# Kernel optimization log

Hardware: AMD Instinct MI355X
Metric: run time of the kernel (lower is better)

Reference implementation:

```python
import jax, jax.numpy as jnp
import numpy as np

K = 10
NEG_SLOPE = 0.2


def _knn(x, k):
    # x: (B, C, N) -> idx (B, N, k) of k nearest neighbors (smallest sq-dist)
    inner = -2.0 * jnp.einsum('bcn,bcm->bnm', x, x)
    xx = jnp.sum(x * x, axis=1)  # (B, N)
    pd = -xx[:, :, None] - inner - xx[:, None, :]  # negative squared distance
    return jax.lax.top_k(pd, k)[1]


def _gather(xt, idx):
    # xt: (B, N, C), idx: (B, N, k) -> (B, N, k, C)
    return jax.vmap(lambda f, i: f[i])(xt, idx)


def graph_feature(x, k):
    # x: (B, C, N) -> (B, 2C, N, k)
    idx = _knn(x, k)
    xt = jnp.transpose(x, (0, 2, 1))  # (B, N, C)
    feat = _gather(xt, idx)           # (B, N, k, C)
    xc = xt[:, :, None, :]
    out = jnp.concatenate([feat - xc, jnp.broadcast_to(xc, feat.shape)], axis=3)
    return jnp.transpose(out, (0, 3, 1, 2))


def graph_feature1(x, k):
    # knn on first 2 dims (2D coords); x: (B, C, N) -> (B, 2C, N, k)
    idx = _knn(x[:, 0:2, :], k)
    xt = jnp.transpose(x, (0, 2, 1))
    feat = _gather(xt, idx)
    xc = jnp.broadcast_to(xt[:, :, None, :], feat.shape)
    out = jnp.concatenate([feat[..., :2] - xc[..., :2], feat[..., 2:], xc], axis=3)
    return jnp.transpose(out, (0, 3, 1, 2))


def _lrelu(v):
    return jnp.where(v >= 0, v, NEG_SLOPE * v)


def _cbr2(f, W, s, t):
    # 1x1 conv2d + folded-BN + leaky relu; f: (B, C, N, k)
    y = jnp.einsum('oc,bcnk->bonk', W, f)
    return _lrelu(y * s[None, :, None, None] + t[None, :, None, None])


def _cbr1(f, W, s, t):
    # 1x1 conv1d + folded-BN + leaky relu; f: (B, C, N)
    y = jnp.einsum('oc,bcn->bon', W, f)
    return _lrelu(y * s[None, :, None] + t[None, :, None])


def setup_inputs() -> dict:
    key = jax.random.key(0)
    ks = jax.random.split(key, 32)
    B, C, N = 8, 7, 4096
    d = {'x': jax.random.normal(ks[0], (B, C, N), jnp.float32)}
    wshapes = [('W1', (64, 14)), ('W2', (64, 64)), ('W3', (64, 128)), ('W4', (64, 64)),
               ('W5', (64, 128)), ('W6', (256, 192)), ('W7', (512, 448)), ('W8', (128, 1024))]
    for i, (n, s) in enumerate(wshapes):
        d[n] = jax.random.normal(ks[1 + i], s, jnp.float32) * (1.0 / np.sqrt(s[1]))
    bdims = [64, 64, 64, 64, 64, 256, 512, 128]
    for i, c in enumerate(bdims):
        d[f's{i + 1}'] = jax.random.uniform(ks[9 + i], (c,), jnp.float32, 0.5, 1.5)
        d[f't{i + 1}'] = jax.random.normal(ks[17 + i], (c,), jnp.float32) * 0.1
    return d


def reference(x, W1, W2, W3, W4, W5, W6, W7, W8,
              s1, s2, s3, s4, s5, s6, s7, s8,
              t1, t2, t3, t4, t5, t6, t7, t8):
    B, _, N = x.shape
    h = graph_feature1(x, K)              # (B, 14, N, K)
    h = _cbr2(h, W1, s1, t1)
    h = _cbr2(h, W2, s2, t2)
    x1 = h.mean(axis=-1)                  # (B, 64, N)
    h = graph_feature(x1, K)              # (B, 128, N, K)
    h = _cbr2(h, W3, s3, t3)
    h = _cbr2(h, W4, s4, t4)
    x2 = h.mean(axis=-1)
    h = graph_feature(x2, K)
    h = _cbr2(h, W5, s5, t5)
    x3 = h.mean(axis=-1)
    h = jnp.concatenate([x1, x2, x3], axis=1)   # (B, 192, N)
    h = _cbr1(h, W6, s6, t6)                    # (B, 256, N)
    g = h.mean(axis=-1, keepdims=True)          # (B, 256, 1)
    g = jnp.broadcast_to(g, (B, 256, N))
    h = jnp.concatenate([g, x1, x2, x3], axis=1)  # (B, 448, N)
    h = _cbr1(h, W7, s7, t7)                      # (B, 512, N)
    x4 = h.max(axis=-1)
    x5 = h.mean(axis=-1)
    h = jnp.concatenate([x4, x5], axis=1)         # (B, 1024)
    h = h @ W8.T                                  # (B, 128)
    return _lrelu(h * s8[None, :] + t8[None, :])
```

## Files before the change

kernel.cpp:

```cpp
#include <hip/hip_runtime.h>

#define BB 8
#define NN 4096
#define KK 10
#define CAP 24
#define TT 6
typedef unsigned long long u64;
typedef __attribute__((ext_vector_type(8))) short bf16x8;
typedef __attribute__((ext_vector_type(4))) float f32x4;

__device__ __forceinline__ float lrelu(float v){ return v >= 0.f ? v : 0.2f*v; }
__device__ __forceinline__ float bc(float v, int l){
  return __int_as_float(__builtin_amdgcn_readlane(__float_as_int(v), l));
}
__device__ __forceinline__ unsigned fenc(float f){
  unsigned u = __float_as_uint(f);
  return u ^ (((unsigned)((int)u >> 31)) | 0x80000000u);
}
__device__ __forceinline__ float fdec(unsigned e){
  return (e & 0x80000000u) ? __uint_as_float(e & 0x7fffffffu) : __uint_as_float(~e);
}
__device__ __forceinline__ u64 shflx_u64(u64 x, int d){
  unsigned lo = __shfl_xor((unsigned)x, d, 64);
  unsigned hi = __shfl_xor((unsigned)(x >> 32), d, 64);
  return ((u64)hi << 32) | lo;
}

__global__ __launch_bounds__(256) void prep_k(
    const float* __restrict__ W1, const float* __restrict__ W2, const float* __restrict__ W3,
    const float* __restrict__ W4, const float* __restrict__ W5, const float* __restrict__ W8,
    float* __restrict__ W1T, float* __restrict__ W2T, float* __restrict__ W3T,
    float* __restrict__ W4T, float* __restrict__ W5T, float* __restrict__ W8T)
{
  const int t = blockIdx.x*256 + threadIdx.x;
  const int stride = gridDim.x*256;
  for (int i=t; i<64*14; i+=stride){ int o=i/14, c=i%14; W1T[c*64+o]=W1[i]; }
  for (int i=t; i<64*64; i+=stride){ int o=i>>6, c=i&63; W2T[c*64+o]=W2[i]; }
  for (int i=t; i<64*128; i+=stride){ int o=i>>7, c=i&127; W3T[c*64+o]=W3[i]; }
  for (int i=t; i<64*64; i+=stride){ int o=i>>6, c=i&63; W4T[c*64+o]=W4[i]; }
  for (int i=t; i<64*128; i+=stride){ int o=i>>7, c=i&127; W5T[c*64+o]=W5[i]; }
  for (int i=t; i<128*1024; i+=stride){ int o=i>>10, c=i&1023; W8T[c*128+o]=W8[i]; }
}

__global__ __launch_bounds__(256) void cvt_k(const float* __restrict__ xin,
    unsigned short* __restrict__ Xh, unsigned short* __restrict__ Xl, float* __restrict__ xx)
{
  const int gid = blockIdx.x*256 + threadIdx.x;
  const int p = gid >> 3, c8 = (gid & 7) << 3;
  const float* src = xin + (size_t)p*64 + c8;
  float fv[8];
  *(float4*)&fv[0] = *(const float4*)(src);
  *(float4*)&fv[4] = *(const float4*)(src + 4);
  unsigned hp[4], lp[4];
  float ssq = 0.f;
  #pragma unroll
  for (int e=0; e<4; e++){
    float f0 = fv[2*e], f1 = fv[2*e+1];
    ssq += f0*f0 + f1*f1;
    unsigned u0 = __float_as_uint(f0), u1 = __float_as_uint(f1);
    hp[e] = (u0 >> 16) | (u1 & 0xffff0000u);
    float l0 = f0 - __uint_as_float(u0 & 0xffff0000u);
    float l1 = f1 - __uint_as_float(u1 & 0xffff0000u);
    lp[e] = (__float_as_uint(l0) >> 16) | (__float_as_uint(l1) & 0xffff0000u);
  }
  *(uint4*)(Xh + (size_t)p*64 + c8) = uint4{hp[0],hp[1],hp[2],hp[3]};
  *(uint4*)(Xl + (size_t)p*64 + c8) = uint4{lp[0],lp[1],lp[2],lp[3]};
  ssq += __shfl_xor(ssq, 1, 64);
  ssq += __shfl_xor(ssq, 2, 64);
  ssq += __shfl_xor(ssq, 4, 64);
  if ((gid & 7) == 0) xx[p] = ssq;
}

__global__ __launch_bounds__(256) void knn2d_k(const float* __restrict__ x, u64* __restrict__ pk)
{
  __shared__ float px[1024], py[1024], pxx[1024];
  __shared__ unsigned cnt[64];
  __shared__ u64 lst[64][CAP];
  const int tid = threadIdx.x;
  const int b  = blockIdx.x >> 8;
  const int qt = (blockIdx.x >> 2) & 63;
  const int h  = blockIdx.x & 3;
  const int q0 = qt*64;
  const int m0g = h*1024;
  const float* xb = x + (size_t)b*7*NN;
  for (int m = tid; m < 1024; m += 256){
    float a = xb[m0g + m], c = xb[NN + m0g + m];
    px[m] = a; py[m] = c; pxx[m] = a*a + c*c;
  }
  if (tid < 64) cnt[tid] = 0;
  __syncthreads();

  const int ty = tid >> 4, tx = tid & 15;
  const int qr = ty*4;
  float qx4[4], qy4[4], q24[4];
  #pragma unroll
  for (int i=0;i<4;i++){
    float a = xb[q0+qr+i], c = xb[NN + q0+qr+i];
    qx4[i] = a; qy4[i] = c; q24[i] = a*a + c*c;
  }

  float bv[4][TT];
  #pragma unroll
  for (int i=0;i<4;i++){
    #pragma unroll
    for (int s=0;s<TT;s++) bv[i][s] = -__builtin_inff();
  }

  for (int ot=0; ot<8; ot++){
    #pragma unroll
    for (int j=0;j<8;j++){
      const int ml = ot*128 + j*16 + tx;
      const float cmx = px[ml], cmy = py[ml], cm2 = pxx[ml];
      #pragma unroll
      for (int i=0;i<4;i++){
        float dot = qx4[i]*cmx + qy4[i]*cmy;
        float v = (-q24[i]) - (-2.f*dot) - cm2;
        float c = v;
        #pragma unroll
        for (int s=0;s<TT;s++){
          float nb = fmaxf(bv[i][s], c);
          c = fminf(bv[i][s], c);
          bv[i][s] = nb;
        }
      }
    }
  }

  float thr[4];
  #pragma unroll
  for (int i=0;i<4;i++){
    float m = 0.f;
    #pragma unroll
    for (int k=0;k<10;k++){
      float hh = bv[i][0];
      m = hh;
      m = fmaxf(m, __shfl_xor(m, 1, 64));
      m = fmaxf(m, __shfl_xor(m, 2, 64));
      m = fmaxf(m, __shfl_xor(m, 4, 64));
      m = fmaxf(m, __shfl_xor(m, 8, 64));
      if (k < 9){
        if (hh == m){
          #pragma unroll
          for (int s=0;s<TT-1;s++) bv[i][s] = bv[i][s+1];
          bv[i][TT-1] = -__builtin_inff();
        }
      }
    }
    thr[i] = m;
  }

  for (int ot=0; ot<8; ot++){
    #pragma unroll
    for (int j=0;j<8;j++){
      const int ml = ot*128 + j*16 + tx;
      const float cmx = px[ml], cmy = py[ml], cm2 = pxx[ml];
      const unsigned mk = ~(unsigned)(m0g + ml);
      #pragma unroll
      for (int i=0;i<4;i++){
        float dot = qx4[i]*cmx + qy4[i]*cmy;
        float v = (-q24[i]) - (-2.f*dot) - cm2;
        if (v >= thr[i]){
          u64 key = ((u64)fenc(v) << 32) | mk;
          const int r = qr + i;
          unsigned slot = atomicAdd(&cnt[r], 1u);
          if (slot < CAP) lst[r][slot] = key;
        }
      }
    }
  }
  __syncthreads();

  if (tid < 64){
    int n = (int)cnt[tid]; if (n > CAP) n = CAP;
    u64* L = lst[tid];
    u64* op = pk + (((size_t)b*NN + q0 + tid)*4 + h)*KK;
    for (int k=0;k<KK;k++){
      u64 best = 0ull; int bi = 0;
      for (int s=0;s<n;s++){
        u64 v2 = L[s];
        if (v2 > best){ best = v2; bi = s; }
      }
      if (best) L[bi] = 0ull;
      op[k] = best;
    }
  }
}

__global__ __launch_bounds__(256) void knn64_k(const unsigned short* __restrict__ Xh,
    const unsigned short* __restrict__ Xl, const float* __restrict__ xx, u64* __restrict__ pk)
{
  __shared__ unsigned short Ch[64*72], Cl[64*72];
  __shared__ float cxx[64];
  __shared__ unsigned cnt[64];
  __shared__ u64 lst[64][CAP];
  const int tid = threadIdx.x;
  const int b  = blockIdx.x >> 8;
  const int qt = (blockIdx.x >> 2) & 63;
  const int h  = blockIdx.x & 3;
  const int q0 = qt*64;
  const int m0g = h*1024;
  const unsigned short* Xhb = Xh + (size_t)b*NN*64;
  const unsigned short* Xlb = Xl + (size_t)b*NN*64;
  const float* xxb = xx + (size_t)b*NN;

  const int sp = tid >> 2;
  const int sc = (tid & 3) << 4;

  const int lane = tid & 63;
  const int w    = tid >> 6;
  const int col  = lane & 15;
  const int quad = (tid >> 4) & 3;
  const int qr   = (tid >> 4)*4;

  const size_t abase = (size_t)(q0 + w*16 + col)*64 + quad*8;
  bf16x8 Ah0 = *(const bf16x8*)(Xhb + abase);
  bf16x8 Ah1 = *(const bf16x8*)(Xhb + abase + 32);
  bf16x8 Al0 = *(const bf16x8*)(Xlb + abase);
  bf16x8 Al1 = *(const bf16x8*)(Xlb + abase + 32);

  float qx4[4];
  #pragma unroll
  for (int i=0;i<4;i++) qx4[i] = xxb[q0 + qr + i];

  if (tid < 64) cnt[tid] = 0;

  float bv[4][TT];
  #pragma unroll
  for (int i=0;i<4;i++){
    #pragma unroll
    for (int s=0;s<TT;s++) bv[i][s] = -__builtin_inff();
  }

  for (int ct=0; ct<16; ct++){
    const int m0 = m0g + ct*64;
    __syncthreads();
    {
      const uint4* sh = (const uint4*)(Xhb + (size_t)(m0+sp)*64 + sc);
      const uint4* sl = (const uint4*)(Xlb + (size_t)(m0+sp)*64 + sc);
      uint4 h0 = sh[0], h1 = sh[1], l0 = sl[0], l1 = sl[1];
      *(uint4*)(&Ch[sp*72 + sc])     = h0;
      *(uint4*)(&Ch[sp*72 + sc + 8]) = h1;
      *(uint4*)(&Cl[sp*72 + sc])     = l0;
      *(uint4*)(&Cl[sp*72 + sc + 8]) = l1;
      if (tid < 64) cxx[tid] = xxb[m0 + tid];
    }
    __syncthreads();

    #pragma unroll
    for (int j=0;j<4;j++){
      const int boff = (j*16 + col)*72 + quad*8;
      bf16x8 Bh0 = *(const bf16x8*)(&Ch[boff]);
      bf16x8 Bh1 = *(const bf16x8*)(&Ch[boff+32]);
      bf16x8 Bl0 = *(const bf16x8*)(&Cl[boff]);
      bf16x8 Bl1 = *(const bf16x8*)(&Cl[boff+32]);
      f32x4 d = {0.f,0.f,0.f,0.f};
      d = __builtin_amdgcn_mfma_f32_16x16x32_bf16(Al0, Bh0, d, 0,0,0);
      d = __builtin_amdgcn_mfma_f32_16x16x32_bf16(Ah0, Bl0, d, 0,0,0);
      d = __builtin_amdgcn_mfma_f32_16x16x32_bf16(Ah0, Bh0, d, 0,0,0);
      d = __builtin_amdgcn_mfma_f32_16x16x32_bf16(Al1, Bh1, d, 0,0,0);
      d = __builtin_amdgcn_mfma_f32_16x16x32_bf16(Ah1, Bl1, d, 0,0,0);
      d = __builtin_amdgcn_mfma_f32_16x16x32_bf16(Ah1, Bh1, d, 0,0,0);

      const float cx = cxx[j*16 + col];
      #pragma unroll
      for (int i=0;i<4;i++){
        float v = (-qx4[i]) - (-2.f*d[i]) - cx;
        float c = v;
        #pragma unroll
        for (int s=0;s<TT;s++){
          float nb = fmaxf(bv[i][s], c);
          c = fminf(bv[i][s], c);
          bv[i][s] = nb;
        }
      }
    }
  }

  float thr[4];
  #pragma unroll
  for (int i=0;i<4;i++){
    float m = 0.f;
    #pragma unroll
    for (int k=0;k<10;k++){
      float hh = bv[i][0];
      m = hh;
      m = fmaxf(m, __shfl_xor(m, 1, 64));
      m = fmaxf(m, __shfl_xor(m, 2, 64));
      m = fmaxf(m, __shfl_xor(m, 4, 64));
      m = fmaxf(m, __shfl_xor(m, 8, 64));
      if (k < 9){
        if (hh == m){
          #pragma unroll
          for (int s=0;s<TT-1;s++) bv[i][s] = bv[i][s+1];
          bv[i][TT-1] = -__builtin_inff();
        }
      }
    }
    thr[i] = m;
  }

  for (int ct=0; ct<16; ct++){
    const int m0 = m0g + ct*64;
    __syncthreads();
    {
      const uint4* sh = (const uint4*)(Xhb + (size_t)(m0+sp)*64 + sc);
      const uint4* sl = (const uint4*)(Xlb + (size_t)(m0+sp)*64 + sc);
      uint4 h0 = sh[0], h1 = sh[1], l0 = sl[0], l1 = sl[1];
      *(uint4*)(&Ch[sp*72 + sc])     = h0;
      *(uint4*)(&Ch[sp*72 + sc + 8]) = h1;
      *(uint4*)(&Cl[sp*72 + sc])     = l0;
      *(uint4*)(&Cl[sp*72 + sc + 8]) = l1;
      if (tid < 64) cxx[tid] = xxb[m0 + tid];
    }
    __syncthreads();

    #pragma unroll
    for (int j=0;j<4;j++){
      const int boff = (j*16 + col)*72 + quad*8;
      bf16x8 Bh0 = *(const bf16x8*)(&Ch[boff]);
      bf16x8 Bh1 = *(const bf16x8*)(&Ch[boff+32]);
      bf16x8 Bl0 = *(const bf16x8*)(&Cl[boff]);
      bf16x8 Bl1 = *(const bf16x8*)(&Cl[boff+32]);
      f32x4 d = {0.f,0.f,0.f,0.f};
      d = __builtin_amdgcn_mfma_f32_16x16x32_bf16(Al0, Bh0, d, 0,0,0);
      d = __builtin_amdgcn_mfma_f32_16x16x32_bf16(Ah0, Bl0, d, 0,0,0);
      d = __builtin_amdgcn_mfma_f32_16x16x32_bf16(Ah0, Bh0, d, 0,0,0);
      d = __builtin_amdgcn_mfma_f32_16x16x32_bf16(Al1, Bh1, d, 0,0,0);
      d = __builtin_amdgcn_mfma_f32_16x16x32_bf16(Ah1, Bl1, d, 0,0,0);
      d = __builtin_amdgcn_mfma_f32_16x16x32_bf16(Ah1, Bh1, d, 0,0,0);

      const int m = m0 + j*16 + col;
      const float cx = cxx[j*16 + col];
      const unsigned mk = ~(unsigned)m;
      #pragma unroll
      for (int i=0;i<4;i++){
        float v = (-qx4[i]) - (-2.f*d[i]) - cx;
        if (v >= thr[i]){
          u64 key = ((u64)fenc(v) << 32) | mk;
          const int r = qr + i;
          unsigned slot = atomicAdd(&cnt[r], 1u);
          if (slot < CAP) lst[r][slot] = key;
        }
      }
    }
  }
  __syncthreads();

  if (tid < 64){
    int n = (int)cnt[tid]; if (n > CAP) n = CAP;
    u64* L = lst[tid];
    u64* op = pk + (((size_t)b*NN + q0 + tid)*4 + h)*KK;
    for (int k=0;k<KK;k++){
      u64 best = 0ull; int bi = 0;
      for (int s=0;s<n;s++){
        u64 v2 = L[s];
        if (v2 > best){ best = v2; bi = s; }
      }
      if (best) L[bi] = 0ull;
      op[k] = best;
    }
  }
}

__global__ __launch_bounds__(256) void kmerge_k(const u64* __restrict__ pk, int* __restrict__ idxo)
{
  const int q = blockIdx.x*256 + threadIdx.x;
  const u64* A = pk + (size_t)q*(4*KK);
  int* op = idxo + (size_t)q*KK;
  int ia = 0, ib = 0, ic = 0, id = 0;
  #pragma unroll
  for (int k=0;k<KK;k++){
    u64 a  = (ia < KK) ? A[ia]        : 0ull;
    u64 b2 = (ib < KK) ? A[KK + ib]   : 0ull;
    u64 c2 = (ic < KK) ? A[2*KK + ic] : 0ull;
    u64 d2 = (id < KK) ? A[3*KK + id] : 0ull;
    u64 m1 = a >= b2 ? a : b2;  int s1 = a >= b2 ? 0 : 1;
    u64 m2 = c2 >= d2 ? c2 : d2; int s2 = c2 >= d2 ? 2 : 3;
    u64 mm = m1 >= m2 ? m1 : m2; int ss = m1 >= m2 ? s1 : s2;
    op[k] = (int)(~(unsigned)mm);
    if (ss == 0) ia++; else if (ss == 1) ib++; else if (ss == 2) ic++; else id++;
  }
}

__global__ __launch_bounds__(256) void edge1_k(const float* __restrict__ x, const int* __restrict__ idx,
    const float* __restrict__ W1T, const float* __restrict__ W2T,
    const float* __restrict__ s1, const float* __restrict__ t1,
    const float* __restrict__ s2, const float* __restrict__ t2,
    float* __restrict__ x1t)
{
  const int lane = threadIdx.x & 63;
  const int pt = (blockIdx.x << 2) + (threadIdx.x >> 6);
  const int b = pt >> 12, n = pt & 4095;
  const float* xb = x + (size_t)b*7*NN;
  float w1r[14], w2r[64];
  #pragma unroll
  for (int c=0;c<14;c++) w1r[c] = W1T[c*64 + lane];
  #pragma unroll
  for (int c=0;c<64;c++) w2r[c] = W2T[c*64 + lane];
  const float s1o=s1[lane], t1o=t1[lane], s2o=s2[lane], t2o=t2[lane];
  const float xq = (lane < 7) ? xb[lane*NN + n] : 0.f;
  const float xq0 = bc(xq,0), xq1 = bc(xq,1);
  float qy1 = 0.f;
  #pragma unroll
  for (int c=0;c<7;c++) qy1 += w1r[7+c]*bc(xq,c);
  const int* ip = idx + (size_t)pt*KK;
  float acc = 0.f;
  for (int j=0;j<KK;j++){
    const int ij = ip[j];
    const float xg = (lane < 7) ? xb[lane*NN + ij] : 0.f;
    float y1 = qy1;
    y1 += w1r[0]*(bc(xg,0) - xq0);
    y1 += w1r[1]*(bc(xg,1) - xq1);
    #pragma unroll
    for (int c=2;c<7;c++) y1 += w1r[c]*bc(xg,c);
    const float z1 = lrelu(y1*s1o + t1o);
    float p0=0.f,p1=0.f,p2=0.f,p3=0.f;
    #pragma unroll
    for (int c=0;c<64;c+=4){
      p0 += w2r[c+0]*bc(z1,c+0);
      p1 += w2r[c+1]*bc(z1,c+1);
      p2 += w2r[c+2]*bc(z1,c+2);
      p3 += w2r[c+3]*bc(z1,c+3);
    }
    acc += lrelu(((p0+p1)+(p2+p3))*s2o + t2o);
  }
  x1t[(size_t)pt*64 + lane] = acc / 10.f;
}

__global__ __launch_bounds__(256) void edge2_k(const float* __restrict__ xin, const int* __restrict__ idx,
    const float* __restrict__ W3T, const float* __restrict__ W4T,
    const float* __restrict__ s3, const float* __restrict__ t3,
    const float* __restrict__ s4, const float* __restrict__ t4,
    float* __restrict__ xout)
{
  const int lane = threadIdx.x & 63;
  const int pt = (blockIdx.x << 2) + (threadIdx.x >> 6);
  const int b = pt >> 12;
  float wd[64], wq[64], w4[64];
  #pragma unroll
  for (int c=0;c<64;c++) wd[c] = W3T[c*64 + lane];
  #pragma unroll
  for (int c=0;c<64;c++) wq[c] = W3T[(64+c)*64 + lane];
  #pragma unroll
  for (int c=0;c<64;c++) w4[c] = W4T[c*64 + lane];
  const float s3o=s3[lane], t3o=t3[lane], s4o=s4[lane], t4o=t4[lane];
  const float xq = xin[(size_t)pt*64 + lane];
  float a0=0.f,a1=0.f,a2=0.f,a3=0.f;
  #pragma unroll
  for (int c=0;c<64;c+=4){
    a0 += wq[c+0]*bc(xq,c+0);
    a1 += wq[c+1]*bc(xq,c+1);
    a2 += wq[c+2]*bc(xq,c+2);
    a3 += wq[c+3]*bc(xq,c+3);
  }
  const float yq = (a0+a1)+(a2+a3);
  const int* ip = idx + (size_t)pt*KK;
  float acc = 0.f;
  for (int j=0;j<KK;j++){
    const int ij = ip[j];
    const float xg = xin[((size_t)(b*NN + ij))*64 + lane];
    const float d = xg - xq;
    float p0=0.f,p1=0.f,p2=0.f,p3=0.f;
    #pragma unroll
    for (int c=0;c<64;c+=4){
      p0 += wd[c+0]*bc(d,c+0);
      p1 += wd[c+1]*bc(d,c+1);
      p2 += wd[c+2]*bc(d,c+2);
      p3 += wd[c+3]*bc(d,c+3);
    }
    const float z3 = lrelu((yq + ((p0+p1)+(p2+p3)))*s3o + t3o);
    float q0=0.f,q1=0.f,q2=0.f,q3=0.f;
    #pragma unroll
    for (int c=0;c<64;c+=4){
      q0 += w4[c+0]*bc(z3,c+0);
      q1 += w4[c+1]*bc(z3,c+1);
      q2 += w4[c+2]*bc(z3,c+2);
      q3 += w4[c+3]*bc(z3,c+3);
    }
    acc += lrelu(((q0+q1)+(q2+q3))*s4o + t4o);
  }
  xout[(size_t)pt*64 + lane] = acc / 10.f;
}

__global__ __launch_bounds__(256) void edge3_k(const float* __restrict__ xin, const int* __restrict__ idx,
    const float* __restrict__ W5T,
    const float* __restrict__ s5, const float* __restrict__ t5,
    float* __restrict__ xout)
{
  const int lane = threadIdx.x & 63;
  const int pt = (blockIdx.x << 2) + (threadIdx.x >> 6);
  const int b = pt >> 12;
  float wd[64], wq[64];
  #pragma unroll
  for (int c=0;c<64;c++) wd[c] = W5T[c*64 + lane];
  #pragma unroll
  for (int c=0;c<64;c++) wq[c] = W5T[(64+c)*64 + lane];
  const float s5o=s5[lane], t5o=t5[lane];
  const float xq = xin[(size_t)pt*64 + lane];
  float a0=0.f,a1=0.f,a2=0.f,a3=0.f;
  #pragma unroll
  for (int c=0;c<64;c+=4){
    a0 += wq[c+0]*bc(xq,c+0);
    a1 += wq[c+1]*bc(xq,c+1);
    a2 += wq[c+2]*bc(xq,c+2);
    a3 += wq[c+3]*bc(xq,c+3);
  }
  const float yq = (a0+a1)+(a2+a3);
  const int* ip = idx + (size_t)pt*KK;
  float acc = 0.f;
  for (int j=0;j<KK;j++){
    const int ij = ip[j];
    const float xg = xin[((size_t)(b*NN + ij))*64 + lane];
    const float d = xg - xq;
    float p0=0.f,p1=0.f,p2=0.f,p3=0.f;
    #pragma unroll
    for (int c=0;c<64;c+=4){
      p0 += wd[c+0]*bc(d,c+0);
      p1 += wd[c+1]*bc(d,c+1);
      p2 += wd[c+2]*bc(d,c+2);
      p3 += wd[c+3]*bc(d,c+3);
    }
    acc += lrelu((yq + ((p0+p1)+(p2+p3)))*s5o + t5o);
  }
  xout[(size_t)pt*64 + lane] = acc / 10.f;
}

__global__ __launch_bounds__(256) void g1_k(const float* __restrict__ W6,
   const float* __restrict__ x1t, const float* __restrict__ x2t, const float* __restrict__ x3t,
   const float* __restrict__ s6, const float* __restrict__ t6, float* __restrict__ gsum)
{
  __shared__ float Wl[16*132];
  __shared__ float Zl[16*260];
  const int tid = threadIdx.x;
  const int rb = blockIdx.x & 1;
  const int nt = (blockIdx.x >> 1) & 15;
  const int b  = blockIdx.x >> 5;
  const int r0 = rb*128;
  const int n0 = nt*256;
  const int ty = tid >> 4, tx = tid & 15;
  float acc[8][16];
  #pragma unroll
  for (int i=0;i<8;i++){
    #pragma unroll
    for (int j=0;j<16;j++) acc[i][j] = 0.f;
  }
  for (int kc=0; kc<12; kc++){
    __syncthreads();
    {
      const int r = tid >> 1, h = tid & 1;
      const float4* wp = (const float4*)(W6 + (size_t)(r0 + r)*192 + kc*16 + h*8);
      float tmp[8];
      *(float4*)&tmp[0] = wp[0];
      *(float4*)&tmp[4] = wp[1];
      #pragma unroll
      for (int u=0;u<8;u++) Wl[(h*8+u)*132 + r] = tmp[u];
    }
    {
      const float* arr = (kc < 4) ? x1t : (kc < 8) ? x2t : x3t;
      const int chofs = (kc & 3)*16;
      const float4* zp = (const float4*)(arr + ((size_t)(b*NN) + n0 + tid)*64 + chofs);
      float tmp[16];
      *(float4*)&tmp[0]  = zp[0];
      *(float4*)&tmp[4]  = zp[1];
      *(float4*)&tmp[8]  = zp[2];
      *(float4*)&tmp[12] = zp[3];
      #pragma unroll
      for (int u=0;u<16;u++) Zl[u*260 + tid] = tmp[u];
    }
    __syncthreads();
    #pragma unroll 4
    for (int k=0;k<16;k++){
      float wv[8], zv[16];
      *(float4*)&wv[0] = *(const float4*)(&Wl[k*132 + ty*8]);
      *(float4*)&wv[4] = *(const float4*)(&Wl[k*132 + ty*8 + 4]);
      #pragma unroll
      for (int jg=0;jg<4;jg++)
        *(float4*)&zv[jg*4] = *(const float4*)(&Zl[k*260 + jg*64 + tx*4]);
      #pragma unroll
      for (int i=0;i<8;i++){
        #pragma unroll
        for (int j=0;j<16;j++) acc[i][j] += wv[i]*zv[j];
      }
    }
  }
  #pragma unroll
  for (int i=0;i<8;i++){
    const int row = r0 + ty*8 + i;
    const float sv = s6[row], tv = t6[row];
    float sum = 0.f;
    #pragma unroll
    for (int j=0;j<16;j++) sum += lrelu(acc[i][j]*sv + tv);
    #pragma unroll
    for (int d=1; d<16; d<<=1) sum += __shfl_xor(sum, d, 64);
    if ((tid & 15) == 0) atomicAdd(&gsum[b*256 + row], sum);
  }
}

__global__ __launch_bounds__(256) void g2_k(const float* __restrict__ W7,
   const float* __restrict__ gsum, float* __restrict__ c7)
{
  const int b = blockIdx.x >> 1;
  const int o = (blockIdx.x & 1)*256 + threadIdx.x;
  const float* wr = W7 + (size_t)o*448;
  const float* gb = gsum + b*256;
  float a0=0.f,a1=0.f,a2=0.f,a3=0.f;
  #pragma unroll 4
  for (int c=0;c<256;c+=4){
    a0 += wr[c+0]*gb[c+0]; a1 += wr[c+1]*gb[c+1];
    a2 += wr[c+2]*gb[c+2]; a3 += wr[c+3]*gb[c+3];
  }
  c7[b*512+o] = ((a0+a1)+(a2+a3)) * (1.f/4096.f);
}

__global__ __launch_bounds__(256) void g3_k(const float* __restrict__ W7,
   const float* __restrict__ x1t, const float* __restrict__ x2t, const float* __restrict__ x3t,
   const float* __restrict__ c7, const float* __restrict__ s7, const float* __restrict__ t7,
   unsigned* __restrict__ x4e, float* __restrict__ x5s)
{
  __shared__ float Wl[16*132];
  __shared__ float Zl[16*260];
  const int tid = threadIdx.x;
  const int rb = blockIdx.x & 3;
  const int nt = (blockIdx.x >> 2) & 15;
  const int b  = blockIdx.x >> 6;
  const int r0 = rb*128;
  const int n0 = nt*256;
  const int ty = tid >> 4, tx = tid & 15;
  float acc[8][16];
  #pragma unroll
  for (int i=0;i<8;i++){
    #pragma unroll
    for (int j=0;j<16;j++) acc[i][j] = 0.f;
  }
  for (int kc=0; kc<12; kc++){
    __syncthreads();
    {
      const int r = tid >> 1, h = tid & 1;
      const float4* wp = (const float4*)(W7 + (size_t)(r0 + r)*448 + 256 + kc*16 + h*8);
      float tmp[8];
      *(float4*)&tmp[0] = wp[0];
      *(float4*)&tmp[4] = wp[1];
      #pragma unroll
      for (int u=0;u<8;u++) Wl[(h*8+u)*132 + r] = tmp[u];
    }
    {
      const float* arr = (kc < 4) ? x1t : (kc < 8) ? x2t : x3t;
      const int chofs = (kc & 3)*16;
      const float4* zp = (const float4*)(arr + ((size_t)(b*NN) + n0 + tid)*64 + chofs);
      float tmp[16];
      *(float4*)&tmp[0]  = zp[0];
      *(float4*)&tmp[4]  = zp[1];
      *(float4*)&tmp[8]  = zp[2];
      *(float4*)&tmp[12] = zp[3];
      #pragma unroll
      for (int u=0;u<16;u++) Zl[u*260 + tid] = tmp[u];
    }
    __syncthreads();
    #pragma unroll 4
    for (int k=0;k<16;k++){
      float wv[8], zv[16];
      *(float4*)&wv[0] = *(const float4*)(&Wl[k*132 + ty*8]);
      *(float4*)&wv[4] = *(const float4*)(&Wl[k*132 + ty*8 + 4]);
      #pragma unroll
      for (int jg=0;jg<4;jg++)
        *(float4*)&zv[jg*4] = *(const float4*)(&Zl[k*260 + jg*64 + tx*4]);
      #pragma unroll
      for (int i=0;i<8;i++){
        #pragma unroll
        for (int j=0;j<16;j++) acc[i][j] += wv[i]*zv[j];
      }
    }
  }
  #pragma unroll
  for (int i=0;i<8;i++){
    const int row = r0 + ty*8 + i;
    const float c7v = c7[b*512 + row];
    const float sv = s7[row], tv = t7[row];
    float mx = -__builtin_inff(), sum = 0.f;
    #pragma unroll
    for (int j=0;j<16;j++){
      float h = lrelu((acc[i][j] + c7v)*sv + tv);
      mx = fmaxf(mx, h); sum += h;
    }
    #pragma unroll
    for (int d=1; d<16; d<<=1){
      sum += __shfl_xor(sum, d, 64);
      mx = fmaxf(mx, __shfl_xor(mx, d, 64));
    }
    if ((tid & 15) == 0){
      atomicAdd(&x5s[b*512 + row], sum);
      atomicMax(&x4e[b*512 + row], fenc(mx));
    }
  }
}

__global__ __launch_bounds__(128) void g4_k(const float* __restrict__ W8T,
  const unsigned* __restrict__ x4e, const float* __restrict__ x5s,
  const float* __restrict__ s8, const float* __restrict__ t8, float* __restrict__ out)
{
  const int b = blockIdx.x, j = threadIdx.x;
  float a0 = 0.f, a1 = 0.f;
  for (int o=0;o<512;o++){
    a0 += W8T[o*128 + j] * fdec(x4e[b*512 + o]);
    a1 += W8T[(512+o)*128 + j] * (x5s[b*512 + o] * (1.f/4096.f));
  }
  const float y = a0 + a1;
  out[b*128 + j] = lrelu(y*s8[j] + t8[j]);
}

extern "C" void kernel_launch(void* const* d_in, const int* in_sizes, int n_in,
                              void* d_out, int out_size, void* d_ws, size_t ws_size,
                              hipStream_t stream) {
  (void)in_sizes; (void)n_in; (void)out_size; (void)ws_size;
  const float* x  = (const float*)d_in[0];
  const float* W1 = (const float*)d_in[1];
  const float* W2 = (const float*)d_in[2];
  const float* W3 = (const float*)d_in[3];
  const float* W4 = (const float*)d_in[4];
  const float* W5 = (const float*)d_in[5];
  const float* W6 = (const float*)d_in[6];
  const float* W7 = (const float*)d_in[7];
  const float* W8 = (const float*)d_in[8];
  const float* s1 = (const float*)d_in[9];   const float* t1 = (const float*)d_in[10];
  const float* s2 = (const float*)d_in[11];  const float* t2 = (const float*)d_in[12];
  const float* s3 = (const float*)d_in[13];  const float* t3 = (const float*)d_in[14];
  const float* s4 = (const float*)d_in[15];  const float* t4 = (const float*)d_in[16];
  const float* s5 = (const float*)d_in[17];  const float* t5 = (const float*)d_in[18];
  const float* s6 = (const float*)d_in[19];  const float* t6 = (const float*)d_in[20];
  const float* s7 = (const float*)d_in[21];  const float* t7 = (const float*)d_in[22];
  const float* s8 = (const float*)d_in[23];  const float* t8 = (const float*)d_in[24];

  char* wsb = (char*)d_ws;
  size_t off = 0;
  auto alloc = [&](size_t bytes)->char* {
    char* p = wsb + off;
    off += (bytes + 255) & ~(size_t)255;
    return p;
  };
  int*      idx1 = (int*)alloc((size_t)BB*NN*KK*4);
  int*      idx2 = (int*)alloc((size_t)BB*NN*KK*4);
  int*      idx3 = (int*)alloc((size_t)BB*NN*KK*4);
  u64*      pkeys= (u64*)alloc((size_t)BB*NN*4*KK*8);
  float*    x1t  = (float*)alloc((size_t)BB*NN*64*4);
  float*    x2t  = (float*)alloc((size_t)BB*NN*64*4);
  float*    x3t  = (float*)alloc((size_t)BB*NN*64*4);
  unsigned short* Xh = (unsigned short*)alloc((size_t)BB*NN*64*2);
  unsigned short* Xl = (unsigned short*)alloc((size_t)BB*NN*64*2);
  float*    xxb  = (float*)alloc((size_t)BB*NN*4);
  float*    gsum = (float*)alloc((size_t)BB*256*4);
  unsigned* x4e  = (unsigned*)alloc((size_t)BB*512*4);
  float*    x5s  = (float*)alloc((size_t)BB*512*4);
  float*    c7   = (float*)alloc((size_t)BB*512*4);
  float*    W1T  = (float*)alloc(14*64*4);
  float*    W2T  = (float*)alloc(64*64*4);
  float*    W3T  = (float*)alloc(128*64*4);
  float*    W4T  = (float*)alloc(64*64*4);
  float*    W5T  = (float*)alloc(128*64*4);
  float*    W8T  = (float*)alloc(1024*128*4);

  prep_k<<<64,256,0,stream>>>(W1,W2,W3,W4,W5,W8, W1T,W2T,W3T,W4T,W5T,W8T);
  knn2d_k<<<BB*64*4,256,0,stream>>>(x, pkeys);
  kmerge_k<<<BB*NN/256,256,0,stream>>>(pkeys, idx1);
  edge1_k<<<BB*NN/4,256,0,stream>>>(x, idx1, W1T, W2T, s1,t1,s2,t2, x1t);
  cvt_k<<<BB*NN*8/256,256,0,stream>>>(x1t, Xh, Xl, xxb);
  knn64_k<<<BB*64*4,256,0,stream>>>(Xh, Xl, xxb, pkeys);
  kmerge_k<<<BB*NN/256,256,0,stream>>>(pkeys, idx2);
  edge2_k<<<BB*NN/4,256,0,stream>>>(x1t, idx2, W3T, W4T, s3,t3,s4,t4, x2t);
  cvt_k<<<BB*NN*8/256,256,0,stream>>>(x2t, Xh, Xl, xxb);
  knn64_k<<<BB*64*4,256,0,stream>>>(Xh, Xl, xxb, pkeys);
  kmerge_k<<<BB*NN/256,256,0,stream>>>(pkeys, idx3);
  edge3_k<<<BB*NN/4,256,0,stream>>>(x2t, idx3, W5T, s5,t5, x3t);
  hipMemsetAsync(gsum, 0, (size_t)BB*256*4 + (size_t)BB*512*4*2, stream);
  g1_k<<<256,256,0,stream>>>(W6, x1t,x2t,x3t, s6,t6, gsum);
  g2_k<<<16,256,0,stream>>>(W7, gsum, c7);
  g3_k<<<512,256,0,stream>>>(W7, x1t,x2t,x3t, c7, s7,t7, x4e, x5s);
  g4_k<<<BB,128,0,stream>>>(W8T, x4e, x5s, s8,t8, (float*)d_out);
}
```

Baseline: 1.126 ms.

## Rewrite edge2 kernel with split-bf16 MFMA matmuls over 8-point tiles

Replaces the per-lane scalar FMA and readlane broadcast loops in edge2 with MFMA 16x16x32 bf16 matrix multiplies. Weights and gathered edge features are split into high and low bf16 parts (three products each) to keep accuracy close to fp32. Each block now handles 8 points (80 edges) staged in shared memory, and the per-point mean is formed with shared-memory atomics. This removes the 192-float per-thread weight registers and the scalar work, at the cost of LDS traffic, extra barriers and a small loss of precision from dropping the low-times-low term.

```diff
diff --git a/kernel.cpp b/kernel.cpp
--- a/kernel.cpp
+++ b/kernel.cpp
@@ -29,17 +29,40 @@
 __global__ __launch_bounds__(256) void prep_k(
     const float* __restrict__ W1, const float* __restrict__ W2, const float* __restrict__ W3,
     const float* __restrict__ W4, const float* __restrict__ W5, const float* __restrict__ W8,
-    float* __restrict__ W1T, float* __restrict__ W2T, float* __restrict__ W3T,
-    float* __restrict__ W4T, float* __restrict__ W5T, float* __restrict__ W8T)
+    float* __restrict__ W1T, float* __restrict__ W2T, float* __restrict__ W5T, float* __restrict__ W8T,
+    unsigned short* __restrict__ W3dh, unsigned short* __restrict__ W3dl,
+    unsigned short* __restrict__ W3qh, unsigned short* __restrict__ W3ql,
+    unsigned short* __restrict__ W4h,  unsigned short* __restrict__ W4l)
 {
   const int t = blockIdx.x*256 + threadIdx.x;
   const int stride = gridDim.x*256;
   for (int i=t; i<64*14; i+=stride){ int o=i/14, c=i%14; W1T[c*64+o]=W1[i]; }
   for (int i=t; i<64*64; i+=stride){ int o=i>>6, c=i&63; W2T[c*64+o]=W2[i]; }
-  for (int i=t; i<64*128; i+=stride){ int o=i>>7, c=i&127; W3T[c*64+o]=W3[i]; }
-  for (int i=t; i<64*64; i+=stride){ int o=i>>6, c=i&63; W4T[c*64+o]=W4[i]; }
   for (int i=t; i<64*128; i+=stride){ int o=i>>7, c=i&127; W5T[c*64+o]=W5[i]; }
   for (int i=t; i<128*1024; i+=stride){ int o=i>>10, c=i&1023; W8T[c*128+o]=W8[i]; }
+  for (int i=t; i<64*64; i+=stride){
+    int o=i>>6, c=i&63;
+    float f = W3[o*128 + c];
+    unsigned u = __float_as_uint(f);
+    W3dh[i] = (unsigned short)(u >> 16);
+    float lo = f - __uint_as_float(u & 0xffff0000u);
+    W3dl[i] = (unsigned short)(__float_as_uint(lo) >> 16);
+  }
+  for (int i=t; i<64*64; i+=stride){
+    int o=i>>6, c=i&63;
+    float f = W3[o*128 + 64 + c];
+    unsigned u = __float_as_uint(f);
+    W3qh[i] = (unsigned short)(u >> 16);
+    float lo = f - __uint_as_float(u & 0xffff0000u);
+    W3ql[i] = (unsigned short)(__float_as_uint(lo) >> 16);
+  }
+  for (int i=t; i<64*64; i+=stride){
+    float f = W4[i];
+    unsigned u = __float_as_uint(f);
+    W4h[i] = (unsigned short)(u >> 16);
+    float lo = f - __uint_as_float(u & 0xffff0000u);
+    W4l[i] = (unsigned short)(__float_as_uint(lo) >> 16);
+  }
 }
 
 __global__ __launch_bounds__(256) void cvt_k(const float* __restrict__ xin,
@@ -427,59 +450,206 @@
   x1t[(size_t)pt*64 + lane] = acc / 10.f;
 }
 
-__global__ __launch_bounds__(256) void edge2_k(const float* __restrict__ xin, const int* __restrict__ idx,
-    const float* __restrict__ W3T, const float* __restrict__ W4T,
+__global__ __launch_bounds__(256) void edge2_k(const float* __restrict__ x1t, const int* __restrict__ idx,
+    const unsigned short* __restrict__ W3dh, const unsigned short* __restrict__ W3dl,
+    const unsigned short* __restrict__ W3qh, const unsigned short* __restrict__ W3ql,
+    const unsigned short* __restrict__ W4h,  const unsigned short* __restrict__ W4l,
     const float* __restrict__ s3, const float* __restrict__ t3,
     const float* __restrict__ s4, const float* __restrict__ t4,
     float* __restrict__ xout)
 {
-  const int lane = threadIdx.x & 63;
-  const int pt = (blockIdx.x << 2) + (threadIdx.x >> 6);
-  const int b = pt >> 12;
-  float wd[64], wq[64], w4[64];
-  #pragma unroll
-  for (int c=0;c<64;c++) wd[c] = W3T[c*64 + lane];
-  #pragma unroll
-  for (int c=0;c<64;c++) wq[c] = W3T[(64+c)*64 + lane];
-  #pragma unroll
-  for (int c=0;c<64;c++) w4[c] = W4T[c*64 + lane];
-  const float s3o=s3[lane], t3o=t3[lane], s4o=s4[lane], t4o=t4[lane];
-  const float xq = xin[(size_t)pt*64 + lane];
-  float a0=0.f,a1=0.f,a2=0.f,a3=0.f;
-  #pragma unroll
-  for (int c=0;c<64;c+=4){
-    a0 += wq[c+0]*bc(xq,c+0);
-    a1 += wq[c+1]*bc(xq,c+1);
-    a2 += wq[c+2]*bc(xq,c+2);
-    a3 += wq[c+3]*bc(xq,c+3);
-  }
-  const float yq = (a0+a1)+(a2+a3);
-  const int* ip = idx + (size_t)pt*KK;
-  float acc = 0.f;
-  for (int j=0;j<KK;j++){
-    const int ij = ip[j];
-    const float xg = xin[((size_t)(b*NN + ij))*64 + lane];
-    const float d = xg - xq;
-    float p0=0.f,p1=0.f,p2=0.f,p3=0.f;
-    #pragma unroll
-    for (int c=0;c<64;c+=4){
-      p0 += wd[c+0]*bc(d,c+0);
-      p1 += wd[c+1]*bc(d,c+1);
-      p2 += wd[c+2]*bc(d,c+2);
-      p3 += wd[c+3]*bc(d,c+3);
-    }
-    const float z3 = lrelu((yq + ((p0+p1)+(p2+p3)))*s3o + t3o);
-    float q0=0.f,q1=0.f,q2=0.f,q3=0.f;
-    #pragma unroll
-    for (int c=0;c<64;c+=4){
-      q0 += w4[c+0]*bc(z3,c+0);
-      q1 += w4[c+1]*bc(z3,c+1);
-      q2 += w4[c+2]*bc(z3,c+2);
-      q3 += w4[c+3]*bc(z3,c+3);
-    }
-    acc += lrelu(((q0+q1)+(q2+q3))*s4o + t4o);
-  }
-  xout[(size_t)pt*64 + lane] = acc / 10.f;
+  __shared__ unsigned short Zh[80*72], Zl[80*72];
+  __shared__ unsigned short Qh[16*72], Ql[16*72];
+  __shared__ float accf[64*8];
+  const int tid = threadIdx.x;
+  const size_t p0 = (size_t)blockIdx.x * 8;
+
+  ((float2*)accf)[tid] = float2{0.f, 0.f};
+
+  #pragma unroll
+  for (int pass=0; pass<2; ++pass){
+    const int col = pass*64 + (tid>>2);
+    const int sc16 = (tid&3)*16;
+    if (col < 88){
+      float dv[16];
+      if (col < 80){
+        const int p = col/10, j = col - p*10;
+        const size_t pt = p0 + p;
+        const int bb = (int)(pt >> 12);
+        const int ij = idx[pt*KK + j];
+        const float* gs = x1t + ((size_t)bb*NN + ij)*64 + sc16;
+        const float* qs = x1t + pt*64 + sc16;
+        #pragma unroll
+        for (int e=0;e<4;e++){
+          float4 g4 = *(const float4*)(gs + e*4);
+          float4 q4 = *(const float4*)(qs + e*4);
+          dv[e*4+0]=g4.x-q4.x; dv[e*4+1]=g4.y-q4.y; dv[e*4+2]=g4.z-q4.z; dv[e*4+3]=g4.w-q4.w;
+        }
+      } else {
+        const int cl = col - 80;
+        const float* qs = x1t + (size_t)(p0+cl)*64 + sc16;
+        #pragma unroll
+        for (int e=0;e<4;e++){
+          float4 q4 = *(const float4*)(qs + e*4);
+          dv[e*4+0]=q4.x; dv[e*4+1]=q4.y; dv[e*4+2]=q4.z; dv[e*4+3]=q4.w;
+        }
+      }
+      unsigned hp[8], lp[8];
+      #pragma unroll
+      for (int e=0;e<8;e++){
+        float f0 = dv[2*e], f1 = dv[2*e+1];
+        unsigned u0 = __float_as_uint(f0), u1 = __float_as_uint(f1);
+        hp[e] = (u0 >> 16) | (u1 & 0xffff0000u);
+        float l0 = f0 - __uint_as_float(u0 & 0xffff0000u);
+        float l1 = f1 - __uint_as_float(u1 & 0xffff0000u);
+        lp[e] = (__float_as_uint(l0) >> 16) | (__float_as_uint(l1) & 0xffff0000u);
+      }
+      if (col < 80){
+        *(uint4*)(&Zh[col*72 + sc16])     = uint4{hp[0],hp[1],hp[2],hp[3]};
+        *(uint4*)(&Zh[col*72 + sc16 + 8]) = uint4{hp[4],hp[5],hp[6],hp[7]};
+        *(uint4*)(&Zl[col*72 + sc16])     = uint4{lp[0],lp[1],lp[2],lp[3]};
+        *(uint4*)(&Zl[col*72 + sc16 + 8]) = uint4{lp[4],lp[5],lp[6],lp[7]};
+      } else {
+        const int cl = col - 80;
+        *(uint4*)(&Qh[cl*72 + sc16])     = uint4{hp[0],hp[1],hp[2],hp[3]};
+        *(uint4*)(&Qh[cl*72 + sc16 + 8]) = uint4{hp[4],hp[5],hp[6],hp[7]};
+        *(uint4*)(&Ql[cl*72 + sc16])     = uint4{lp[0],lp[1],lp[2],lp[3]};
+        *(uint4*)(&Ql[cl*72 + sc16 + 8]) = uint4{lp[4],lp[5],lp[6],lp[7]};
+      }
+    } else if (col < 96){
+      const int cl = col - 80;
+      const uint4 z{0u,0u,0u,0u};
+      *(uint4*)(&Qh[cl*72 + sc16])     = z;
+      *(uint4*)(&Qh[cl*72 + sc16 + 8]) = z;
+      *(uint4*)(&Ql[cl*72 + sc16])     = z;
+      *(uint4*)(&Ql[cl*72 + sc16 + 8]) = z;
+    }
+  }
+  __syncthreads();
+
+  const int lane = tid & 63;
+  const int w    = tid >> 6;
+  const int colL = lane & 15;
+  const int quad = lane >> 4;
+  const int arow = (w*16 + colL)*64 + quad*8;
+
+  bf16x8 Adh0 = *(const bf16x8*)(W3dh + arow);
+  bf16x8 Adh1 = *(const bf16x8*)(W3dh + arow + 32);
+  bf16x8 Adl0 = *(const bf16x8*)(W3dl + arow);
+  bf16x8 Adl1 = *(const bf16x8*)(W3dl + arow + 32);
+
+  f32x4 C1[5];
+  #pragma unroll
+  for (int t=0;t<5;t++){
+    const int boff = (t*16 + colL)*72 + quad*8;
+    bf16x8 Bh0 = *(const bf16x8*)(&Zh[boff]);
+    bf16x8 Bh1 = *(const bf16x8*)(&Zh[boff+32]);
+    bf16x8 Bl0 = *(const bf16x8*)(&Zl[boff]);
+    bf16x8 Bl1 = *(const bf16x8*)(&Zl[boff+32]);
+    f32x4 d = {0.f,0.f,0.f,0.f};
+    d = __builtin_amdgcn_mfma_f32_16x16x32_bf16(Adl0, Bh0, d, 0,0,0);
+    d = __builtin_amdgcn_mfma_f32_16x16x32_bf16(Adh0, Bl0, d, 0,0,0);
+    d = __builtin_amdgcn_mfma_f32_16x16x32_bf16(Adh0, Bh0, d, 0,0,0);
+    d = __builtin_amdgcn_mfma_f32_16x16x32_bf16(Adl1, Bh1, d, 0,0,0);
+    d = __builtin_amdgcn_mfma_f32_16x16x32_bf16(Adh1, Bl1, d, 0,0,0);
+    d = __builtin_amdgcn_mfma_f32_16x16x32_bf16(Adh1, Bh1, d, 0,0,0);
+    C1[t] = d;
+  }
+  f32x4 Cu;
+  {
+    bf16x8 Aqh0 = *(const bf16x8*)(W3qh + arow);
+    bf16x8 Aqh1 = *(const bf16x8*)(W3qh + arow + 32);
+    bf16x8 Aql0 = *(const bf16x8*)(W3ql + arow);
+    bf16x8 Aql1 = *(const bf16x8*)(W3ql + arow + 32);
+    const int boff = colL*72 + quad*8;
+    bf16x8 Bh0 = *(const bf16x8*)(&Qh[boff]);
+    bf16x8 Bh1 = *(const bf16x8*)(&Qh[boff+32]);
+    bf16x8 Bl0 = *(const bf16x8*)(&Ql[boff]);
+    bf16x8 Bl1 = *(const bf16x8*)(&Ql[boff+32]);
+    f32x4 d = {0.f,0.f,0.f,0.f};
+    d = __builtin_amdgcn_mfma_f32_16x16x32_bf16(Aql0, Bh0, d, 0,0,0);
+    d = __builtin_amdgcn_mfma_f32_16x16x32_bf16(Aqh0, Bl0, d, 0,0,0);
+    d = __builtin_amdgcn_mfma_f32_16x16x32_bf16(Aqh0, Bh0, d, 0,0,0);
+    d = __builtin_amdgcn_mfma_f32_16x16x32_bf16(Aql1, Bh1, d, 0,0,0);
+    d = __builtin_amdgcn_mfma_f32_16x16x32_bf16(Aqh1, Bl1, d, 0,0,0);
+    d = __builtin_amdgcn_mfma_f32_16x16x32_bf16(Aqh1, Bh1, d, 0,0,0);
+    Cu = d;
+  }
+
+  float s3v[4], t3v[4], s4v[4], t4v[4];
+  #pragma unroll
+  for (int i=0;i<4;i++){
+    const int o = w*16 + quad*4 + i;
+    s3v[i]=s3[o]; t3v[i]=t3[o]; s4v[i]=s4[o]; t4v[i]=t4[o];
+  }
+
+  __syncthreads();
+
+  #pragma unroll
+  for (int t=0;t<5;t++){
+    const int gc = t*16 + colL;
+    const int p  = gc/10;
+    const int srcb = (((lane & 48) | p) << 2);
+    float z[4];
+    #pragma unroll
+    for (int i=0;i<4;i++){
+      float ui = __int_as_float(__builtin_amdgcn_ds_bpermute(srcb, __float_as_int(Cu[i])));
+      float zp = (C1[t][i] + ui)*s3v[i] + t3v[i];
+      z[i] = zp >= 0.f ? zp : 0.2f*zp;
+    }
+    unsigned u0=__float_as_uint(z[0]), u1=__float_as_uint(z[1]);
+    unsigned u2=__float_as_uint(z[2]), u3=__float_as_uint(z[3]);
+    unsigned h01 = (u0>>16) | (u1 & 0xffff0000u);
+    unsigned h23 = (u2>>16) | (u3 & 0xffff0000u);
+    float l0 = z[0]-__uint_as_float(u0&0xffff0000u);
+    float l1 = z[1]-__uint_as_float(u1&0xffff0000u);
+    float l2 = z[2]-__uint_as_float(u2&0xffff0000u);
+    float l3 = z[3]-__uint_as_float(u3&0xffff0000u);
+    unsigned l01 = (__float_as_uint(l0)>>16) | (__float_as_uint(l1)&0xffff0000u);
+    unsigned l23 = (__float_as_uint(l2)>>16) | (__float_as_uint(l3)&0xffff0000u);
+    const int rb = w*16 + quad*4;
+    *(uint2*)(&Zh[gc*72 + rb]) = uint2{h01,h23};
+    *(uint2*)(&Zl[gc*72 + rb]) = uint2{l01,l23};
+  }
+  __syncthreads();
+
+  bf16x8 A4h0 = *(const bf16x8*)(W4h + arow);
+  bf16x8 A4h1 = *(const bf16x8*)(W4h + arow + 32);
+  bf16x8 A4l0 = *(const bf16x8*)(W4l + arow);
+  bf16x8 A4l1 = *(const bf16x8*)(W4l + arow + 32);
+  #pragma unroll
+  for (int t=0;t<5;t++){
+    const int boff = (t*16 + colL)*72 + quad*8;
+    bf16x8 Bh0 = *(const bf16x8*)(&Zh[boff]);
+    bf16x8 Bh1 = *(const bf16x8*)(&Zh[boff+32]);
+    bf16x8 Bl0 = *(const bf16x8*)(&Zl[boff]);
+    bf16x8 Bl1 = *(const bf16x8*)(&Zl[boff+32]);
+    f32x4 d = {0.f,0.f,0.f,0.f};
+    d = __builtin_amdgcn_mfma_f32_16x16x32_bf16(A4l0, Bh0, d, 0,0,0);
+    d = __builtin_amdgcn_mfma_f32_16x16x32_bf16(A4h0, Bl0, d, 0,0,0);
+    d = __builtin_amdgcn_mfma_f32_16x16x32_bf16(A4h0, Bh0, d, 0,0,0);
+    d = __builtin_amdgcn_mfma_f32_16x16x32_bf16(A4l1, Bh1, d, 0,0,0);
+    d = __builtin_amdgcn_mfma_f32_16x16x32_bf16(A4h1, Bl1, d, 0,0,0);
+    d = __builtin_amdgcn_mfma_f32_16x16x32_bf16(A4h1, Bh1, d, 0,0,0);
+    const int gc = t*16 + colL;
+    const int p  = gc/10;
+    #pragma unroll
+    for (int i=0;i<4;i++){
+      float v = d[i]*s4v[i] + t4v[i];
+      v = v >= 0.f ? v : 0.2f*v;
+      atomicAdd(&accf[(w*16 + quad*4 + i)*8 + p], v);
+    }
+  }
+  __syncthreads();
+
+  {
+    const int o = tid & 63;
+    #pragma unroll
+    for (int g=0; g<2; ++g){
+      const int p = (tid>>6) + g*4;
+      xout[(p0+p)*64 + o] = accf[o*8+p] / 10.f;
+    }
+  }
 }
 
 __global__ __launch_bounds__(256) void edge3_k(const float* __restrict__ xin, const int* __restrict__ idx,
@@ -753,19 +923,23 @@
   float*    c7   = (float*)alloc((size_t)BB*512*4);
   float*    W1T  = (float*)alloc(14*64*4);
   float*    W2T  = (float*)alloc(64*64*4);
-  float*    W3T  = (float*)alloc(128*64*4);
-  float*    W4T  = (float*)alloc(64*64*4);
   float*    W5T  = (float*)alloc(128*64*4);
   float*    W8T  = (float*)alloc(1024*128*4);
-
-  prep_k<<<64,256,0,stream>>>(W1,W2,W3,W4,W5,W8, W1T,W2T,W3T,W4T,W5T,W8T);
+  unsigned short* W3dh = (unsigned short*)alloc(64*64*2);
+  unsigned short* W3dl = (unsigned short*)alloc(64*64*2);
+  unsigned short* W3qh = (unsigned short*)alloc(64*64*2);
+  unsigned short* W3ql = (unsigned short*)alloc(64*64*2);
+  unsigned short* W4h  = (unsigned short*)alloc(64*64*2);
+  unsigned short* W4l  = (unsigned short*)alloc(64*64*2);
+
+  prep_k<<<64,256,0,stream>>>(W1,W2,W3,W4,W5,W8, W1T,W2T,W5T,W8T, W3dh,W3dl,W3qh,W3ql,W4h,W4l);
   knn2d_k<<<BB*64*4,256,0,stream>>>(x, pkeys);
   kmerge_k<<<BB*NN/256,256,0,stream>>>(pkeys, idx1);
   edge1_k<<<BB*NN/4,256,0,stream>>>(x, idx1, W1T, W2T, s1,t1,s2,t2, x1t);
   cvt_k<<<BB*NN*8/256,256,0,stream>>>(x1t, Xh, Xl, xxb);
   knn64_k<<<BB*64*4,256,0,stream>>>(Xh, Xl, xxb, pkeys);
   kmerge_k<<<BB*NN/256,256,0,stream>>>(pkeys, idx2);
-  edge2_k<<<BB*NN/4,256,0,stream>>>(x1t, idx2, W3T, W4T, s3,t3,s4,t4, x2t);
+  edge2_k<<<BB*NN/8,256,0,stream>>>(x1t, idx2, W3dh,W3dl,W3qh,W3ql,W4h,W4l, s3,t3,s4,t4, x2t);
   cvt_k<<<BB*NN*8/256,256,0,stream>>>(x2t, Xh, Xl, xxb);
   knn64_k<<<BB*64*4,256,0,stream>>>(Xh, Xl, xxb, pkeys);
   kmerge_k<<<BB*NN/256,256,0,stream>>>(pkeys, idx3);
```

New measurement: 1.106 ms. No clear change (-1.8%).
